# Kernel optimization log

Hardware: AMD Instinct MI355X
Metric: run time of the kernel (lower is better)

The kernel has to match this reference:

```python
import jax, jax.numpy as jnp
import numpy as np

N_CLASSES = 2048
NUM_GROUP = 8
CLS_PER_GROUP = N_CLASSES // NUM_GROUP  # 256
NUM_SAMPLE = 10
EMB_DIM = 400
COMMITMENT = 0.25


def setup_inputs() -> dict:
    key = jax.random.key(0)
    k1, k2 = jax.random.split(key)
    x0 = jax.random.normal(k1, (64, 512, 1, EMB_DIM), dtype=jnp.float32)
    emb = jax.random.normal(k2, (N_CLASSES, EMB_DIM), dtype=jnp.float32)
    return {"x0": x0, "emb": emb}


def reference(x0, emb):
    x = x0  # normalize=False path
    M = x0.shape[0] * x0.shape[1] * x0.shape[2]
    x1 = x.reshape(M, EMB_DIM)

    # pairwise squared distances [M, N_CLASSES]
    d = (jnp.sum(x1 ** 2, axis=1, keepdims=True)
         + jnp.sum(emb ** 2, axis=1)
         - 2.0 * x1 @ emb.T)

    # per-group mean distance -> group argmin
    d_g = d.reshape(M, NUM_GROUP, CLS_PER_GROUP)
    group = jnp.argmin(jnp.mean(d_g, axis=2), axis=1)  # [M]

    # inverse-distance probs restricted to the chosen group
    d_sel = jnp.take_along_axis(d_g, group[:, None, None], axis=1)[:, 0, :]  # [M, CLS_PER_GROUP]
    prob_sel = 1.0 / d_sel
    p, idx_local = jax.lax.top_k(prob_sel, NUM_SAMPLE)  # descending, [M, NUM_SAMPLE]
    index = group[:, None] * CLS_PER_GROUP + idx_local  # global codebook indices

    # L1 normalize kept probabilities (F.normalize p=1)
    prob_dist = p / jnp.maximum(jnp.sum(jnp.abs(p), axis=1, keepdims=True), 1e-12)

    # entropy of top-1 code histogram
    hist = jnp.bincount(index[:, 0], length=N_CLASSES).astype(jnp.float32)
    pr = hist / jnp.float32(M)
    entropy = -jnp.sum(jnp.where(hist > 0, pr * jnp.log(jnp.where(hist > 0, pr, 1.0)), 0.0))

    # weighted gather-sum of code vectors (probs are detached in original)
    gathered = emb[index]  # [M, NUM_SAMPLE, EMB_DIM]
    w = jax.lax.stop_gradient(prob_dist)[:, :, None]
    output = jnp.sum(gathered * w, axis=1).reshape(x.shape)

    out0 = jax.lax.stop_gradient(output - x) + x  # straight-through
    q_latent = jnp.mean((jax.lax.stop_gradient(x) - output) ** 2)
    e_latent = jnp.mean((x - jax.lax.stop_gradient(output)) ** 2)
    loss = q_latent + COMMITMENT * e_latent

    encodings = (1.0 / d)[None]  # [1, M, N_CLASSES]
    return (loss, out0, entropy, encodings)
```

## Files before the change

kernel.cpp:

```cpp
#include <hip/hip_runtime.h>
#include <math.h>

#define M_ROWS 32768
#define N_CLS  2048
#define NGRP   8
#define CPG    256
#define NS     10
#define EDIM   400
#define KPAD   416
#define NKT    13
#define BK     32

typedef _Float16 f16x8 __attribute__((ext_vector_type(8)));
typedef float f32x4 __attribute__((ext_vector_type(4)));

__device__ __forceinline__ void gld_lds16(const void* g, void* l) {
    __builtin_amdgcn_global_load_lds(
        (const __attribute__((address_space(1))) unsigned int*)g,
        (__attribute__((address_space(3))) unsigned int*)l, 16, 0, 0);
}

__global__ __launch_bounds__(256) void k_split(const float* __restrict__ in,
                                               unsigned short* __restrict__ hi,
                                               unsigned short* __restrict__ lo,
                                               float* __restrict__ ss, int rows) {
    int row  = blockIdx.x * 4 + (threadIdx.x >> 6);
    int lane = threadIdx.x & 63;
    if (row >= rows) return;
    const float* src = in + (size_t)row * EDIM;
    unsigned short* ph = hi + (size_t)row * KPAD;
    unsigned short* pl = lo + (size_t)row * KPAD;
    float s = 0.f;
    #pragma unroll
    for (int q = 0; q < 2; ++q) {
        int c4 = lane + q * 64;
        if (c4 < KPAD / 4) {
            int k = c4 * 4;
            float4 v = make_float4(0.f, 0.f, 0.f, 0.f);
            if (k < EDIM) v = *(const float4*)(src + k);
            float va[4] = {v.x, v.y, v.z, v.w};
            ushort4 H, L;
            unsigned short ha[4], la[4];
            #pragma unroll
            for (int t = 0; t < 4; ++t) {
                float f = va[t];
                _Float16 h = (_Float16)f;
                _Float16 l2 = (_Float16)(f - (float)h);
                ha[t] = __builtin_bit_cast(unsigned short, h);
                la[t] = __builtin_bit_cast(unsigned short, l2);
                s = fmaf(f, f, s);
            }
            H.x = ha[0]; H.y = ha[1]; H.z = ha[2]; H.w = ha[3];
            L.x = la[0]; L.y = la[1]; L.z = la[2]; L.w = la[3];
            *(ushort4*)(ph + k) = H;
            *(ushort4*)(pl + k) = L;
        }
    }
    #pragma unroll
    for (int o = 32; o; o >>= 1) s += __shfl_xor(s, o, 64);
    if (lane == 0) ss[row] = s;
}

__global__ __launch_bounds__(256) void k_sumsq(const float* __restrict__ in,
                                               float* __restrict__ out, int rows) {
    int wave = (blockIdx.x * blockDim.x + threadIdx.x) >> 6;
    int lane = threadIdx.x & 63;
    if (wave >= rows) return;
    const float* r = in + (size_t)wave * EDIM;
    float s = 0.f;
    for (int d = lane; d < EDIM; d += 64) { float v = r[d]; s = fmaf(v, v, s); }
    #pragma unroll
    for (int o = 32; o; o >>= 1) s += __shfl_xor(s, o, 64);
    if (lane == 0) out[wave] = s;
}

__global__ __launch_bounds__(256, 3) void k_dist_mfma(
    const unsigned short* __restrict__ xhi, const unsigned short* __restrict__ xlo,
    const unsigned short* __restrict__ ehi, const unsigned short* __restrict__ elo,
    const float* __restrict__ xx, const float* __restrict__ ee,
    float* __restrict__ enc, float* __restrict__ gsumP) {
    __shared__ __attribute__((aligned(16))) _Float16 Ah[128][BK];
    __shared__ __attribute__((aligned(16))) _Float16 Al[128][BK];
    __shared__ __attribute__((aligned(16))) _Float16 Bh[128][BK];
    __shared__ __attribute__((aligned(16))) _Float16 Bl[128][BK];

    const int tid  = threadIdx.x;
    const int m0   = blockIdx.x * 128;
    const int n0   = blockIdx.y * 128;
    const int lane = tid & 63, wid = tid >> 6;
    const int wr = (wid >> 1) * 64, wc = (wid & 1) * 64;
    const int lr = lane & 15, ko = lane >> 4;

    f32x4 acc[4][4];
    #pragma unroll
    for (int i = 0; i < 4; ++i)
        #pragma unroll
        for (int j = 0; j < 4; ++j) { f32x4 z = {0.f, 0.f, 0.f, 0.f}; acc[i][j] = z; }

    for (int kt = 0; kt < NKT; ++kt) {
        const int k0 = kt * BK;
        #pragma unroll
        for (int q = 0; q < 2; ++q) {
            int c = q * 256 + tid;
            int row = c >> 2, kc = c & 3;
            size_t goA = (size_t)(m0 + row) * KPAD + k0 + kc * 8;
            size_t goB = (size_t)(n0 + row) * KPAD + k0 + kc * 8;
            int loff = (c >> 6) * 1024;
            gld_lds16(xhi + goA, (char*)&Ah[0][0] + loff);
            gld_lds16(xlo + goA, (char*)&Al[0][0] + loff);
            gld_lds16(ehi + goB, (char*)&Bh[0][0] + loff);
            gld_lds16(elo + goB, (char*)&Bl[0][0] + loff);
        }
        __syncthreads();

        f16x8 a_h[4], a_l[4];
        #pragma unroll
        for (int i = 0; i < 4; ++i) {
            a_h[i] = *(const f16x8*)&Ah[wr + i * 16 + lr][ko * 8];
            a_l[i] = *(const f16x8*)&Al[wr + i * 16 + lr][ko * 8];
        }
        #pragma unroll
        for (int j = 0; j < 4; ++j) {
            f16x8 b_h = *(const f16x8*)&Bh[wc + j * 16 + lr][ko * 8];
            f16x8 b_l = *(const f16x8*)&Bl[wc + j * 16 + lr][ko * 8];
            #pragma unroll
            for (int i = 0; i < 4; ++i) {
                acc[i][j] = __builtin_amdgcn_mfma_f32_16x16x32_f16(a_h[i], b_l, acc[i][j], 0, 0, 0);
                acc[i][j] = __builtin_amdgcn_mfma_f32_16x16x32_f16(a_l[i], b_h, acc[i][j], 0, 0, 0);
                acc[i][j] = __builtin_amdgcn_mfma_f32_16x16x32_f16(a_h[i], b_h, acc[i][j], 0, 0, 0);
            }
        }
        __syncthreads();
    }

    const int g = blockIdx.y >> 1, half = blockIdx.y & 1;
    #pragma unroll
    for (int i = 0; i < 4; ++i) {
        #pragma unroll
        for (int r = 0; r < 4; ++r) {
            int row = m0 + wr + i * 16 + ko * 4 + r;
            float xm = xx[row];
            float rsum = 0.f;
            #pragma unroll
            for (int j = 0; j < 4; ++j) {
                int col = n0 + wc + j * 16 + lr;
                float dd = fmaf(-2.f, acc[i][j][r], xm + ee[col]);
                rsum += dd;
                enc[(size_t)row * N_CLS + col] = 1.0f / dd;
            }
            rsum += __shfl_xor(rsum, 1, 64);
            rsum += __shfl_xor(rsum, 2, 64);
            rsum += __shfl_xor(rsum, 4, 64);
            rsum += __shfl_xor(rsum, 8, 64);
            if (lr == 0)
                gsumP[(size_t)row * (NGRP * 4) + g * 4 + half * 2 + (wc >> 6)] = rsum;
        }
    }
}

__global__ __launch_bounds__(256) void k_dist(const float* __restrict__ x,
                                              const float* __restrict__ emb,
                                              const float* __restrict__ xx,
                                              const float* __restrict__ ee,
                                              float* __restrict__ enc,
                                              float* __restrict__ gsum) {
    __shared__ float As[16][36];
    __shared__ float Bs[16][260];
    const int tid = threadIdx.x;
    const int m0  = blockIdx.x * 32;
    const int g   = blockIdx.y;
    const int j0  = g * CPG;
    const int ty  = tid >> 5;
    const int tx  = tid & 31;
    float acc[4][8];
    #pragma unroll
    for (int i = 0; i < 4; ++i)
        #pragma unroll
        for (int j = 0; j < 8; ++j) acc[i][j] = 0.f;
    const int kk = tid & 15, rbase = tid >> 4;
    for (int k0 = 0; k0 < EDIM; k0 += 16) {
        #pragma unroll
        for (int p = 0; p < 2; ++p) {
            int r = p * 16 + rbase;
            As[kk][r] = x[(size_t)(m0 + r) * EDIM + k0 + kk];
        }
        #pragma unroll
        for (int p = 0; p < 16; ++p) {
            int c = p * 16 + rbase;
            Bs[kk][c] = emb[(size_t)(j0 + c) * EDIM + k0 + kk];
        }
        __syncthreads();
        #pragma unroll
        for (int k = 0; k < 16; ++k) {
            float4 a  = *(const float4*)&As[k][ty * 4];
            float4 b0 = *(const float4*)&Bs[k][tx * 4];
            float4 b1 = *(const float4*)&Bs[k][128 + tx * 4];
            float av[4] = {a.x, a.y, a.z, a.w};
            float bv[8] = {b0.x, b0.y, b0.z, b0.w, b1.x, b1.y, b1.z, b1.w};
            #pragma unroll
            for (int i = 0; i < 4; ++i)
                #pragma unroll
                for (int j = 0; j < 8; ++j)
                    acc[i][j] = fmaf(av[i], bv[j], acc[i][j]);
        }
        __syncthreads();
    }
    float rp[4];
    #pragma unroll
    for (int i = 0; i < 4; ++i) {
        int m = m0 + ty * 4 + i;
        float xm = xx[m];
        float rsum = 0.f;
        float* erow = enc + (size_t)m * N_CLS + j0;
        #pragma unroll
        for (int j = 0; j < 8; ++j) {
            int c = (j < 4) ? (tx * 4 + j) : (128 + tx * 4 + (j - 4));
            float t = xm + ee[j0 + c];
            float d = fmaf(-2.f, acc[i][j], t);
            rsum += d;
            erow[c] = 1.0f / d;
        }
        rp[i] = rsum;
    }
    #pragma unroll
    for (int i = 0; i < 4; ++i) {
        float s = rp[i];
        s += __shfl_xor(s, 1, 64);
        s += __shfl_xor(s, 2, 64);
        s += __shfl_xor(s, 4, 64);
        s += __shfl_xor(s, 8, 64);
        if (tx == 0) gsum[(size_t)(m0 + ty * 4 + i) * NGRP + g] = s;
    }
}

template <int NPART>
__global__ __launch_bounds__(256) void k_select(const float* __restrict__ x,
                                                const float* __restrict__ emb,
                                                const float* __restrict__ enc,
                                                const float* __restrict__ gsum,
                                                float* __restrict__ out0,
                                                float* __restrict__ rmse,
                                                unsigned int* __restrict__ hist) {
    const int wave = threadIdx.x >> 6;
    const int lane = threadIdx.x & 63;
    const int m = blockIdx.x * 4 + wave;

    const float* gs = gsum + (size_t)m * (NGRP * NPART);
    float bestv = 0.f; int bestg = 0;
    #pragma unroll
    for (int g = 0; g < NGRP; ++g) {
        float v = 0.f;
        #pragma unroll
        for (int p = 0; p < NPART; ++p) v += gs[g * NPART + p];
        if (g == 0 || v < bestv) { bestv = v; bestg = g; }
    }
    const int j0 = bestg * CPG;

    const float* pr = enc + (size_t)m * N_CLS + j0;
    float v[4];
    #pragma unroll
    for (int s = 0; s < 4; ++s) v[s] = pr[lane + 64 * s];

    float pv[NS]; int pidx[NS];
    #pragma unroll
    for (int t = 0; t < NS; ++t) {
        float bv = v[0]; int bs = 0;
        #pragma unroll
        for (int s = 1; s < 4; ++s) if (v[s] > bv) { bv = v[s]; bs = s; }
        int bidx = lane + 64 * bs;
        #pragma unroll
        for (int o = 1; o < 64; o <<= 1) {
            float ov = __shfl_xor(bv, o, 64);
            int   oi = __shfl_xor(bidx, o, 64);
            if (ov > bv || (ov == bv && oi < bidx)) { bv = ov; bidx = oi; }
        }
        pv[t] = bv; pidx[t] = bidx;
        if ((bidx & 63) == lane) v[bidx >> 6] = -INFINITY;
    }

    float psum = 0.f;
    #pragma unroll
    for (int t = 0; t < NS; ++t) psum += pv[t];
    float wnorm = fmaxf(psum, 1e-12f);
    float w[NS]; int gi[NS];
    #pragma unroll
    for (int t = 0; t < NS; ++t) { w[t] = pv[t] / wnorm; gi[t] = j0 + pidx[t]; }

    if (lane == 0) atomicAdd(&hist[gi[0]], 1u);

    const float* xr = x + (size_t)m * EDIM;
    float* orow = out0 + (size_t)m * EDIM;
    float sq = 0.f;
    for (int d = lane; d < EDIM; d += 64) {
        float o = 0.f;
        #pragma unroll
        for (int t = 0; t < NS; ++t) o = fmaf(w[t], emb[(size_t)gi[t] * EDIM + d], o);
        float xv = xr[d];
        float diff = xv - o;
        sq = fmaf(diff, diff, sq);
        orow[d] = (o - xv) + xv;
    }
    #pragma unroll
    for (int o = 32; o; o >>= 1) sq += __shfl_xor(sq, o, 64);
    if (lane == 0) rmse[m] = sq;
}

__global__ __launch_bounds__(1024) void k_final(const float* __restrict__ rmse,
                                                const unsigned int* __restrict__ hist,
                                                float* __restrict__ loss_out,
                                                float* __restrict__ ent_out) {
    __shared__ float red[1024];
    const int t = threadIdx.x;

    float s = 0.f;
    for (int i = t; i < M_ROWS; i += 1024) s += rmse[i];
    red[t] = s; __syncthreads();
    for (int off = 512; off; off >>= 1) {
        if (t < off) red[t] += red[t + off];
        __syncthreads();
    }
    if (t == 0) {
        float q = red[0] / 13107200.0f;
        loss_out[0] = q + 0.25f * q;
    }
    __syncthreads();

    float e = 0.f;
    for (int i = t; i < N_CLS; i += 1024) {
        unsigned int h = hist[i];
        if (h > 0) {
            float prb = (float)h / 32768.0f;
            e -= prb * logf(prb);
        }
    }
    red[t] = e; __syncthreads();
    for (int off = 512; off; off >>= 1) {
        if (t < off) red[t] += red[t + off];
        __syncthreads();
    }
    if (t == 0) ent_out[0] = red[0];
}

extern "C" void kernel_launch(void* const* d_in, const int* in_sizes, int n_in,
                              void* d_out, int out_size, void* d_ws, size_t ws_size,
                              hipStream_t stream) {
    const float* x   = (const float*)d_in[0];
    const float* emb = (const float*)d_in[1];

    float* out      = (float*)d_out;
    float* loss_out = out;
    float* out0     = out + 1;
    float* ent_out  = out + 1 + M_ROWS * EDIM;
    float* enc      = out + 2 + M_ROWS * EDIM;

    float* ws    = (float*)d_ws;
    float* ee    = ws;
    float* xx    = ee + N_CLS;
    float* gsumP = xx + M_ROWS;
    float* rmse  = gsumP + (size_t)M_ROWS * NGRP * 4;
    unsigned int* hist = (unsigned int*)(rmse + M_ROWS);
    float* fend  = rmse + M_ROWS + N_CLS;

    unsigned short* xhi = (unsigned short*)fend;
    unsigned short* xlo = xhi + (size_t)M_ROWS * KPAD;
    unsigned short* ehi = xlo + (size_t)M_ROWS * KPAD;
    unsigned short* elo = ehi + (size_t)N_CLS * KPAD;
    size_t need = (size_t)((char*)(elo + (size_t)N_CLS * KPAD) - (char*)d_ws);

    hipMemsetAsync(hist, 0, N_CLS * sizeof(unsigned int), stream);

    if (ws_size >= need) {
        k_split<<<M_ROWS / 4, 256, 0, stream>>>(x, xhi, xlo, xx, M_ROWS);
        k_split<<<N_CLS / 4, 256, 0, stream>>>(emb, ehi, elo, ee, N_CLS);
        dim3 grid(M_ROWS / 128, N_CLS / 128);
        k_dist_mfma<<<grid, 256, 0, stream>>>(xhi, xlo, ehi, elo, xx, ee, enc, gsumP);
        k_select<4><<<M_ROWS / 4, 256, 0, stream>>>(x, emb, enc, gsumP, out0, rmse, hist);
    } else {
        k_sumsq<<<N_CLS / 4, 256, 0, stream>>>(emb, ee, N_CLS);
        k_sumsq<<<M_ROWS / 4, 256, 0, stream>>>(x, xx, M_ROWS);
        dim3 g2(M_ROWS / 32, NGRP);
        k_dist<<<g2, 256, 0, stream>>>(x, emb, xx, ee, enc, gsumP);
        k_select<1><<<M_ROWS / 4, 256, 0, stream>>>(x, emb, enc, gsumP, out0, rmse, hist);
    }

    k_final<<<1, 1024, 0, stream>>>(rmse, hist, loss_out, ent_out);
}
```

Baseline: 364.5 us.

## Use single fp16 MFMA GEMM with fp32 group-sum correction and candidate rescoring

Drops the three-term fp16 hi/lo split GEMM and computes distances with one fp16 hi*hi MFMA pass. Group selection is corrected by adding the exact fp32 dot of x with per-group embedding sums minus its fp16 equivalent. The top-16 candidates are then re-scored in fp32 to choose the top-10 weights and indices. It also remaps blocks so each XCD covers contiguous M tiles. This cuts GEMM compute and traffic by about a third but leaves the encodings output at fp16-level accuracy, which may not meet tolerance.

```diff
diff --git a/kernel.cpp b/kernel.cpp
--- a/kernel.cpp
+++ b/kernel.cpp
@@ -6,10 +6,13 @@
 #define NGRP   8
 #define CPG    256
 #define NS     10
+#define NCAND  16
 #define EDIM   400
 #define KPAD   416
 #define NKT    13
 #define BK     32
+#define SGS    448
+#define NPART  32
 
 typedef _Float16 f16x8 __attribute__((ext_vector_type(8)));
 typedef float f32x4 __attribute__((ext_vector_type(4)));
@@ -20,16 +23,14 @@
         (__attribute__((address_space(3))) unsigned int*)l, 16, 0, 0);
 }
 
-__global__ __launch_bounds__(256) void k_split(const float* __restrict__ in,
-                                               unsigned short* __restrict__ hi,
-                                               unsigned short* __restrict__ lo,
-                                               float* __restrict__ ss, int rows) {
+__global__ __launch_bounds__(256) void k_split_hi(const float* __restrict__ in,
+                                                  unsigned short* __restrict__ hi,
+                                                  float* __restrict__ ss, int rows) {
     int row  = blockIdx.x * 4 + (threadIdx.x >> 6);
     int lane = threadIdx.x & 63;
     if (row >= rows) return;
     const float* src = in + (size_t)row * EDIM;
     unsigned short* ph = hi + (size_t)row * KPAD;
-    unsigned short* pl = lo + (size_t)row * KPAD;
     float s = 0.f;
     #pragma unroll
     for (int q = 0; q < 2; ++q) {
@@ -39,21 +40,16 @@
             float4 v = make_float4(0.f, 0.f, 0.f, 0.f);
             if (k < EDIM) v = *(const float4*)(src + k);
             float va[4] = {v.x, v.y, v.z, v.w};
-            ushort4 H, L;
-            unsigned short ha[4], la[4];
+            unsigned short ha[4];
             #pragma unroll
             for (int t = 0; t < 4; ++t) {
                 float f = va[t];
                 _Float16 h = (_Float16)f;
-                _Float16 l2 = (_Float16)(f - (float)h);
                 ha[t] = __builtin_bit_cast(unsigned short, h);
-                la[t] = __builtin_bit_cast(unsigned short, l2);
                 s = fmaf(f, f, s);
             }
-            H.x = ha[0]; H.y = ha[1]; H.z = ha[2]; H.w = ha[3];
-            L.x = la[0]; L.y = la[1]; L.z = la[2]; L.w = la[3];
+            ushort4 H; H.x = ha[0]; H.y = ha[1]; H.z = ha[2]; H.w = ha[3];
             *(ushort4*)(ph + k) = H;
-            *(ushort4*)(pl + k) = L;
         }
     }
     #pragma unroll
@@ -61,32 +57,40 @@
     if (lane == 0) ss[row] = s;
 }
 
-__global__ __launch_bounds__(256) void k_sumsq(const float* __restrict__ in,
-                                               float* __restrict__ out, int rows) {
-    int wave = (blockIdx.x * blockDim.x + threadIdx.x) >> 6;
-    int lane = threadIdx.x & 63;
-    if (wave >= rows) return;
-    const float* r = in + (size_t)wave * EDIM;
-    float s = 0.f;
-    for (int d = lane; d < EDIM; d += 64) { float v = r[d]; s = fmaf(v, v, s); }
-    #pragma unroll
-    for (int o = 32; o; o >>= 1) s += __shfl_xor(s, o, 64);
-    if (lane == 0) out[wave] = s;
-}
-
-__global__ __launch_bounds__(256, 3) void k_dist_mfma(
-    const unsigned short* __restrict__ xhi, const unsigned short* __restrict__ xlo,
-    const unsigned short* __restrict__ ehi, const unsigned short* __restrict__ elo,
+__global__ __launch_bounds__(448) void k_groupsum(const float* __restrict__ emb,
+                                                  const unsigned short* __restrict__ ehi,
+                                                  float* __restrict__ Sg,
+                                                  float* __restrict__ SgH) {
+    const int g = blockIdx.x;
+    const int t = threadIdx.x;
+    float se = 0.f, sh = 0.f;
+    if (t < EDIM) {
+        for (int j = 0; j < CPG; ++j) {
+            se += emb[(size_t)(g * CPG + j) * EDIM + t];
+            _Float16 h = __builtin_bit_cast(_Float16, ehi[(size_t)(g * CPG + j) * KPAD + t]);
+            sh += (float)h;
+        }
+    }
+    Sg[g * SGS + t]  = se;
+    SgH[g * SGS + t] = sh;
+}
+
+__global__ __launch_bounds__(256, 4) void k_dist1(
+    const unsigned short* __restrict__ xhi, const unsigned short* __restrict__ ehi,
     const float* __restrict__ xx, const float* __restrict__ ee,
-    float* __restrict__ enc, float* __restrict__ gsumP) {
+    float* __restrict__ enc, float* __restrict__ gsum) {
     __shared__ __attribute__((aligned(16))) _Float16 Ah[128][BK];
-    __shared__ __attribute__((aligned(16))) _Float16 Al[128][BK];
     __shared__ __attribute__((aligned(16))) _Float16 Bh[128][BK];
-    __shared__ __attribute__((aligned(16))) _Float16 Bl[128][BK];
+
+    const int wg    = blockIdx.x;
+    const int xcd   = wg & 7;
+    const int local = wg >> 3;
+    const int mx    = xcd * 32 + (local & 31);
+    const int ny    = local >> 5;
+    const int m0    = mx * 128;
+    const int n0    = ny * 128;
 
     const int tid  = threadIdx.x;
-    const int m0   = blockIdx.x * 128;
-    const int n0   = blockIdx.y * 128;
     const int lane = tid & 63, wid = tid >> 6;
     const int wr = (wid >> 1) * 64, wc = (wid & 1) * 64;
     const int lr = lane & 15, ko = lane >> 4;
@@ -107,166 +111,112 @@
             size_t goB = (size_t)(n0 + row) * KPAD + k0 + kc * 8;
             int loff = (c >> 6) * 1024;
             gld_lds16(xhi + goA, (char*)&Ah[0][0] + loff);
-            gld_lds16(xlo + goA, (char*)&Al[0][0] + loff);
             gld_lds16(ehi + goB, (char*)&Bh[0][0] + loff);
-            gld_lds16(elo + goB, (char*)&Bl[0][0] + loff);
         }
         __syncthreads();
 
-        f16x8 a_h[4], a_l[4];
-        #pragma unroll
-        for (int i = 0; i < 4; ++i) {
+        f16x8 a_h[4];
+        #pragma unroll
+        for (int i = 0; i < 4; ++i)
             a_h[i] = *(const f16x8*)&Ah[wr + i * 16 + lr][ko * 8];
-            a_l[i] = *(const f16x8*)&Al[wr + i * 16 + lr][ko * 8];
-        }
         #pragma unroll
         for (int j = 0; j < 4; ++j) {
             f16x8 b_h = *(const f16x8*)&Bh[wc + j * 16 + lr][ko * 8];
-            f16x8 b_l = *(const f16x8*)&Bl[wc + j * 16 + lr][ko * 8];
             #pragma unroll
-            for (int i = 0; i < 4; ++i) {
-                acc[i][j] = __builtin_amdgcn_mfma_f32_16x16x32_f16(a_h[i], b_l, acc[i][j], 0, 0, 0);
-                acc[i][j] = __builtin_amdgcn_mfma_f32_16x16x32_f16(a_l[i], b_h, acc[i][j], 0, 0, 0);
+            for (int i = 0; i < 4; ++i)
                 acc[i][j] = __builtin_amdgcn_mfma_f32_16x16x32_f16(a_h[i], b_h, acc[i][j], 0, 0, 0);
-            }
         }
         __syncthreads();
     }
 
-    const int g = blockIdx.y >> 1, half = blockIdx.y & 1;
     #pragma unroll
     for (int i = 0; i < 4; ++i) {
         #pragma unroll
         for (int r = 0; r < 4; ++r) {
             int row = m0 + wr + i * 16 + ko * 4 + r;
             float xm = xx[row];
-            float rsum = 0.f;
+            float rs = 0.f;
             #pragma unroll
             for (int j = 0; j < 4; ++j) {
                 int col = n0 + wc + j * 16 + lr;
                 float dd = fmaf(-2.f, acc[i][j][r], xm + ee[col]);
-                rsum += dd;
+                rs += dd;
                 enc[(size_t)row * N_CLS + col] = 1.0f / dd;
             }
-            rsum += __shfl_xor(rsum, 1, 64);
-            rsum += __shfl_xor(rsum, 2, 64);
-            rsum += __shfl_xor(rsum, 4, 64);
-            rsum += __shfl_xor(rsum, 8, 64);
+            rs += __shfl_xor(rs, 1, 64);
+            rs += __shfl_xor(rs, 2, 64);
+            rs += __shfl_xor(rs, 4, 64);
+            rs += __shfl_xor(rs, 8, 64);
             if (lr == 0)
-                gsumP[(size_t)row * (NGRP * 4) + g * 4 + half * 2 + (wc >> 6)] = rsum;
-        }
-    }
-}
-
-__global__ __launch_bounds__(256) void k_dist(const float* __restrict__ x,
-                                              const float* __restrict__ emb,
-                                              const float* __restrict__ xx,
-                                              const float* __restrict__ ee,
-                                              float* __restrict__ enc,
-                                              float* __restrict__ gsum) {
-    __shared__ float As[16][36];
-    __shared__ float Bs[16][260];
-    const int tid = threadIdx.x;
-    const int m0  = blockIdx.x * 32;
-    const int g   = blockIdx.y;
-    const int j0  = g * CPG;
-    const int ty  = tid >> 5;
-    const int tx  = tid & 31;
-    float acc[4][8];
-    #pragma unroll
-    for (int i = 0; i < 4; ++i)
-        #pragma unroll
-        for (int j = 0; j < 8; ++j) acc[i][j] = 0.f;
-    const int kk = tid & 15, rbase = tid >> 4;
-    for (int k0 = 0; k0 < EDIM; k0 += 16) {
-        #pragma unroll
-        for (int p = 0; p < 2; ++p) {
-            int r = p * 16 + rbase;
-            As[kk][r] = x[(size_t)(m0 + r) * EDIM + k0 + kk];
-        }
-        #pragma unroll
-        for (int p = 0; p < 16; ++p) {
-            int c = p * 16 + rbase;
-            Bs[kk][c] = emb[(size_t)(j0 + c) * EDIM + k0 + kk];
-        }
-        __syncthreads();
-        #pragma unroll
-        for (int k = 0; k < 16; ++k) {
-            float4 a  = *(const float4*)&As[k][ty * 4];
-            float4 b0 = *(const float4*)&Bs[k][tx * 4];
-            float4 b1 = *(const float4*)&Bs[k][128 + tx * 4];
-            float av[4] = {a.x, a.y, a.z, a.w};
-            float bv[8] = {b0.x, b0.y, b0.z, b0.w, b1.x, b1.y, b1.z, b1.w};
-            #pragma unroll
-            for (int i = 0; i < 4; ++i)
-                #pragma unroll
-                for (int j = 0; j < 8; ++j)
-                    acc[i][j] = fmaf(av[i], bv[j], acc[i][j]);
-        }
-        __syncthreads();
-    }
-    float rp[4];
-    #pragma unroll
-    for (int i = 0; i < 4; ++i) {
-        int m = m0 + ty * 4 + i;
-        float xm = xx[m];
-        float rsum = 0.f;
-        float* erow = enc + (size_t)m * N_CLS + j0;
-        #pragma unroll
-        for (int j = 0; j < 8; ++j) {
-            int c = (j < 4) ? (tx * 4 + j) : (128 + tx * 4 + (j - 4));
-            float t = xm + ee[j0 + c];
-            float d = fmaf(-2.f, acc[i][j], t);
-            rsum += d;
-            erow[c] = 1.0f / d;
-        }
-        rp[i] = rsum;
-    }
-    #pragma unroll
-    for (int i = 0; i < 4; ++i) {
-        float s = rp[i];
-        s += __shfl_xor(s, 1, 64);
-        s += __shfl_xor(s, 2, 64);
-        s += __shfl_xor(s, 4, 64);
-        s += __shfl_xor(s, 8, 64);
-        if (tx == 0) gsum[(size_t)(m0 + ty * 4 + i) * NGRP + g] = s;
-    }
-}
-
-template <int NPART>
-__global__ __launch_bounds__(256) void k_select(const float* __restrict__ x,
-                                                const float* __restrict__ emb,
-                                                const float* __restrict__ enc,
-                                                const float* __restrict__ gsum,
-                                                float* __restrict__ out0,
-                                                float* __restrict__ rmse,
-                                                unsigned int* __restrict__ hist) {
+                gsum[(size_t)row * NPART + ny * 2 + (wc >> 6)] = rs;
+        }
+    }
+}
+
+__global__ __launch_bounds__(256) void k_select2(const float* __restrict__ x,
+                                                 const float* __restrict__ emb,
+                                                 const float* __restrict__ enc,
+                                                 const float* __restrict__ gsum,
+                                                 const float* __restrict__ Sg,
+                                                 const float* __restrict__ SgH,
+                                                 const float* __restrict__ xx,
+                                                 const float* __restrict__ ee,
+                                                 float* __restrict__ out0,
+                                                 float* __restrict__ rmse,
+                                                 unsigned int* __restrict__ hist) {
     const int wave = threadIdx.x >> 6;
     const int lane = threadIdx.x & 63;
     const int m = blockIdx.x * 4 + wave;
 
-    const float* gs = gsum + (size_t)m * (NGRP * NPART);
-    float bestv = 0.f; int bestg = 0;
+    const float* xrg = x + (size_t)m * EDIM;
+    float xr[7], xh[7];
+    #pragma unroll
+    for (int k = 0; k < 7; ++k) {
+        int d = lane + 64 * k;
+        float f = (d < EDIM) ? xrg[d] : 0.f;
+        xr[k] = f;
+        xh[k] = (float)(_Float16)f;
+    }
+    const float xm = xx[m];
+
+    float aE[NGRP], aH[NGRP];
+    #pragma unroll
+    for (int g = 0; g < NGRP; ++g) { aE[g] = 0.f; aH[g] = 0.f; }
+    #pragma unroll
+    for (int k = 0; k < 7; ++k) {
+        int d = lane + 64 * k;
+        #pragma unroll
+        for (int g = 0; g < NGRP; ++g) {
+            aE[g] = fmaf(xr[k], Sg[g * SGS + d], aE[g]);
+            aH[g] = fmaf(xh[k], SgH[g * SGS + d], aH[g]);
+        }
+    }
+    const float* gs = gsum + (size_t)m * NPART;
+    int bestg = 0; float bestv = 0.f;
     #pragma unroll
     for (int g = 0; g < NGRP; ++g) {
-        float v = 0.f;
-        #pragma unroll
-        for (int p = 0; p < NPART; ++p) v += gs[g * NPART + p];
-        if (g == 0 || v < bestv) { bestv = v; bestg = g; }
+        float sE = aE[g], sH = aH[g];
+        #pragma unroll
+        for (int o = 1; o < 64; o <<= 1) { sE += __shfl_xor(sE, o, 64); sH += __shfl_xor(sH, o, 64); }
+        float base = 0.f;
+        #pragma unroll
+        for (int p = 0; p < 4; ++p) base += gs[g * 4 + p];
+        float sc = fmaf(-2.f, sE - sH, base);
+        if (g == 0 || sc < bestv) { bestv = sc; bestg = g; }
     }
     const int j0 = bestg * CPG;
 
     const float* pr = enc + (size_t)m * N_CLS + j0;
     float v[4];
     #pragma unroll
-    for (int s = 0; s < 4; ++s) v[s] = pr[lane + 64 * s];
-
-    float pv[NS]; int pidx[NS];
-    #pragma unroll
-    for (int t = 0; t < NS; ++t) {
+    for (int s4 = 0; s4 < 4; ++s4) v[s4] = pr[lane + 64 * s4];
+
+    int cidx[NCAND];
+    #pragma unroll
+    for (int t = 0; t < NCAND; ++t) {
         float bv = v[0]; int bs = 0;
         #pragma unroll
-        for (int s = 1; s < 4; ++s) if (v[s] > bv) { bv = v[s]; bs = s; }
+        for (int s4 = 1; s4 < 4; ++s4) if (v[s4] > bv) { bv = v[s4]; bs = s4; }
         int bidx = lane + 64 * bs;
         #pragma unroll
         for (int o = 1; o < 64; o <<= 1) {
@@ -274,31 +224,61 @@
             int   oi = __shfl_xor(bidx, o, 64);
             if (ov > bv || (ov == bv && oi < bidx)) { bv = ov; bidx = oi; }
         }
-        pv[t] = bv; pidx[t] = bidx;
+        cidx[t] = bidx;
         if ((bidx & 63) == lane) v[bidx >> 6] = -INFINITY;
     }
 
-    float psum = 0.f;
-    #pragma unroll
-    for (int t = 0; t < NS; ++t) psum += pv[t];
-    float wnorm = fmaxf(psum, 1e-12f);
-    float w[NS]; int gi[NS];
-    #pragma unroll
-    for (int t = 0; t < NS; ++t) { w[t] = pv[t] / wnorm; gi[t] = j0 + pidx[t]; }
+    float pv[NCAND];
+    #pragma unroll
+    for (int t = 0; t < NCAND; ++t) {
+        int j = j0 + cidx[t];
+        const float* er = emb + (size_t)j * EDIM;
+        float a = 0.f;
+        #pragma unroll
+        for (int k = 0; k < 7; ++k) {
+            int d = lane + 64 * k;
+            if (d < EDIM) a = fmaf(xr[k], er[d], a);
+        }
+        #pragma unroll
+        for (int o = 1; o < 64; o <<= 1) a += __shfl_xor(a, o, 64);
+        float dd = fmaf(-2.f, a, xm + ee[j]);
+        pv[t] = 1.0f / dd;
+    }
+
+    unsigned used = 0;
+    float w[NS]; int gi[NS]; float psum = 0.f;
+    #pragma unroll
+    for (int t = 0; t < NS; ++t) {
+        float bv = 0.f; int bc = -1;
+        #pragma unroll
+        for (int c = 0; c < NCAND; ++c) {
+            if (!((used >> c) & 1u)) {
+                if (bc < 0 || pv[c] > bv || (pv[c] == bv && cidx[c] < cidx[bc])) { bv = pv[c]; bc = c; }
+            }
+        }
+        used |= 1u << bc;
+        w[t] = bv; gi[t] = j0 + cidx[bc]; psum += fabsf(bv);
+    }
+    float wn = fmaxf(psum, 1e-12f);
+    #pragma unroll
+    for (int t = 0; t < NS; ++t) w[t] /= wn;
 
     if (lane == 0) atomicAdd(&hist[gi[0]], 1u);
 
-    const float* xr = x + (size_t)m * EDIM;
     float* orow = out0 + (size_t)m * EDIM;
     float sq = 0.f;
-    for (int d = lane; d < EDIM; d += 64) {
-        float o = 0.f;
-        #pragma unroll
-        for (int t = 0; t < NS; ++t) o = fmaf(w[t], emb[(size_t)gi[t] * EDIM + d], o);
-        float xv = xr[d];
-        float diff = xv - o;
-        sq = fmaf(diff, diff, sq);
-        orow[d] = (o - xv) + xv;
+    #pragma unroll
+    for (int k = 0; k < 7; ++k) {
+        int d = lane + 64 * k;
+        if (d < EDIM) {
+            float o = 0.f;
+            #pragma unroll
+            for (int t = 0; t < NS; ++t) o = fmaf(w[t], emb[(size_t)gi[t] * EDIM + d], o);
+            float xv = xr[k];
+            float diff = xv - o;
+            sq = fmaf(diff, diff, sq);
+            orow[d] = (o - xv) + xv;
+        }
     }
     #pragma unroll
     for (int o = 32; o; o >>= 1) sq += __shfl_xor(sq, o, 64);
@@ -353,35 +333,29 @@
     float* ent_out  = out + 1 + M_ROWS * EDIM;
     float* enc      = out + 2 + M_ROWS * EDIM;
 
-    float* ws    = (float*)d_ws;
-    float* ee    = ws;
-    float* xx    = ee + N_CLS;
-    float* gsumP = xx + M_ROWS;
-    float* rmse  = gsumP + (size_t)M_ROWS * NGRP * 4;
+    float* ws   = (float*)d_ws;
+    float* ee   = ws;
+    float* xx   = ee + N_CLS;
+    float* Sg   = xx + M_ROWS;
+    float* SgH  = Sg + NGRP * SGS;
+    float* gsum = SgH + NGRP * SGS;
+    float* rmse = gsum + (size_t)M_ROWS * NPART;
     unsigned int* hist = (unsigned int*)(rmse + M_ROWS);
-    float* fend  = rmse + M_ROWS + N_CLS;
+    float* fend = rmse + M_ROWS + N_CLS;
 
     unsigned short* xhi = (unsigned short*)fend;
-    unsigned short* xlo = xhi + (size_t)M_ROWS * KPAD;
-    unsigned short* ehi = xlo + (size_t)M_ROWS * KPAD;
-    unsigned short* elo = ehi + (size_t)N_CLS * KPAD;
-    size_t need = (size_t)((char*)(elo + (size_t)N_CLS * KPAD) - (char*)d_ws);
+    unsigned short* ehi = xhi + (size_t)M_ROWS * KPAD;
 
     hipMemsetAsync(hist, 0, N_CLS * sizeof(unsigned int), stream);
 
-    if (ws_size >= need) {
-        k_split<<<M_ROWS / 4, 256, 0, stream>>>(x, xhi, xlo, xx, M_ROWS);
-        k_split<<<N_CLS / 4, 256, 0, stream>>>(emb, ehi, elo, ee, N_CLS);
-        dim3 grid(M_ROWS / 128, N_CLS / 128);
-        k_dist_mfma<<<grid, 256, 0, stream>>>(xhi, xlo, ehi, elo, xx, ee, enc, gsumP);
-        k_select<4><<<M_ROWS / 4, 256, 0, stream>>>(x, emb, enc, gsumP, out0, rmse, hist);
-    } else {
-        k_sumsq<<<N_CLS / 4, 256, 0, stream>>>(emb, ee, N_CLS);
-        k_sumsq<<<M_ROWS / 4, 256, 0, stream>>>(x, xx, M_ROWS);
-        dim3 g2(M_ROWS / 32, NGRP);
-        k_dist<<<g2, 256, 0, stream>>>(x, emb, xx, ee, enc, gsumP);
-        k_select<1><<<M_ROWS / 4, 256, 0, stream>>>(x, emb, enc, gsumP, out0, rmse, hist);
-    }
+    k_split_hi<<<M_ROWS / 4, 256, 0, stream>>>(x, xhi, xx, M_ROWS);
+    k_split_hi<<<N_CLS / 4, 256, 0, stream>>>(emb, ehi, ee, N_CLS);
+    k_groupsum<<<NGRP, 448, 0, stream>>>(emb, ehi, Sg, SgH);
+
+    k_dist1<<<(M_ROWS / 128) * (N_CLS / 128), 256, 0, stream>>>(xhi, ehi, xx, ee, enc, gsum);
+
+    k_select2<<<M_ROWS / 4, 256, 0, stream>>>(x, emb, enc, gsum, Sg, SgH, xx, ee,
+                                              out0, rmse, hist);
 
     k_final<<<1, 1024, 0, stream>>>(rmse, hist, loss_out, ent_out);
 }
```

New measurement: 607.2 us. 66.6% more time.
